# Kernel tuning notes

Hardware: AMD Instinct MI355X
Metric: run time of the kernel (lower is better)

The kernel has to match this reference:

```python
import jax, jax.numpy as jnp
import numpy as np

B, J, E, H = 32, 512, 512, 8
HD = E // H
EPS = 1e-7


def log_map0_spatial(x):
    # Lorentz log map at origin o=(1,0,...,0); return spatial (tangent) part.
    x0 = jnp.maximum(x[..., 0], 1.0 + 1e-7)      # [B,J]
    xs = x[..., 1:]                               # [B,J,E]
    nrm = jnp.linalg.norm(xs, axis=-1, keepdims=True)
    theta = jnp.arccosh(x0)[..., None]
    return theta * xs / jnp.maximum(nrm, EPS)


def exp_map0(v_s):
    # Lorentz exp map at origin of tangent vector (0, v_s) -> (cosh|v|, sinh|v| v/|v|).
    nrm = jnp.linalg.norm(v_s, axis=-1, keepdims=True)
    safe = jnp.maximum(nrm, EPS)
    return jnp.concatenate([jnp.cosh(nrm), jnp.sinh(nrm) * v_s / safe], axis=-1)


def setup_inputs() -> dict:
    key = jax.random.key(0)
    ks = jax.random.split(key, 8)
    xs = 0.5 * jax.random.normal(ks[0], (B, J, E), dtype=jnp.float32)
    x0 = jnp.sqrt(1.0 + jnp.sum(xs * xs, axis=-1, keepdims=True))  # valid hyperboloid
    x = jnp.concatenate([x0, xs], axis=-1)                          # [B,J,E+1]
    x_vel = jax.random.normal(ks[1], (B, J, E + 1), dtype=jnp.float32)
    topo_bias = 0.1 * jax.random.normal(ks[2], (J, J), dtype=jnp.float32)
    s = 1.0 / np.sqrt(E)
    W_qkv = jax.random.uniform(ks[3], (3 * E, E), jnp.float32, -s, s)
    W_vproj = jax.random.uniform(ks[4], (E, E), jnp.float32, -s, s)
    W_proj = jax.random.uniform(ks[5], (E, E), jnp.float32, -s, s)
    b_proj = jax.random.uniform(ks[6], (E,), jnp.float32, -s, s)
    return {"x": x, "x_vel": x_vel, "topo_bias": topo_bias,
            "W_qkv": W_qkv, "W_vproj": W_vproj, "W_proj": W_proj, "b_proj": b_proj}


def reference(x, x_vel, topo_bias, W_qkv, W_vproj, W_proj, b_proj):
    # Dropout is inference-mode (identity) for a deterministic reference.
    x_tan = log_map0_spatial(x)                                   # [B,J,E]
    v_tan = x_vel[..., 1:]                                        # [B,J,E]
    qkv = (x_tan @ W_qkv.T).reshape(B, J, 3, H, HD)
    qkv = jnp.transpose(qkv, (2, 0, 3, 1, 4))                     # [3,B,H,J,hd]
    q, k, v = qkv[0], qkv[1], qkv[2]
    k_vel = jnp.transpose((v_tan @ W_vproj.T).reshape(B, J, H, HD), (0, 2, 1, 3))
    k = k + k_vel
    scale = HD ** -0.5
    attn = jnp.einsum('bhqd,bhkd->bhqk', q, k) * scale + topo_bias[None, None]
    attn = jax.nn.softmax(attn, axis=-1)                          # [B,H,J,J]
    z_tan = jnp.einsum('bhqk,bhkd->bhqd', attn, v)
    z_tan = jnp.transpose(z_tan, (0, 2, 1, 3)).reshape(B, J, E)
    z_tan = z_tan @ W_proj.T + b_proj
    z_manifold = exp_map0(z_tan)                                  # [B,J,E+1]
    return (z_manifold, attn, x_tan)
```

## Files before the change

kernel.cpp:

```cpp
#include <hip/hip_runtime.h>
#include <hip/hip_bf16.h>
#include <math.h>

#define Jdim 512
#define Edim 512

typedef short short8 __attribute__((ext_vector_type(8)));
typedef float f32x4 __attribute__((ext_vector_type(4)));
typedef unsigned short u16;
typedef unsigned int u32;

__device__ __forceinline__ u16 f2b(float f) {
    union { float f; u32 u; } v; v.f = f;
    u32 r = (v.u + 0x7FFFu + ((v.u >> 16) & 1u)) >> 16;
    return (u16)r;
}
__device__ __forceinline__ float b2f(u16 u) {
    union { u32 u; float f; } v; v.u = ((u32)u) << 16;
    return v.f;
}

__device__ __forceinline__ void gl_lds16(const void* g, void* l) {
    __builtin_amdgcn_global_load_lds(
        (const __attribute__((address_space(1))) u32*)g,
        (__attribute__((address_space(3))) u32*)l, 16, 0, 0);
}

__global__ __launch_bounds__(256) void convw(
    const float* __restrict__ Wqkv, const float* __restrict__ Wvp,
    const float* __restrict__ Wproj,
    u16* __restrict__ Wq, u16* __restrict__ Wv, u16* __restrict__ Wp,
    u16* __restrict__ Wcat)
{
    int i = blockIdx.x * 256 + threadIdx.x;
    if (i < 262144) {
        Wq[i] = f2b(Wqkv[i]);
        Wv[i] = f2b(Wqkv[524288 + i]);
        Wp[i] = f2b(Wproj[i]);
    }
    int n = i >> 10, c = i & 1023;
    float v = (c < 512) ? Wqkv[(size_t)(512 + n) * 512 + c]
                        : Wvp[(size_t)n * 512 + (c - 512)];
    Wcat[i] = f2b(v);
}

__global__ __launch_bounds__(256) void xtan_kernel(
    const float* __restrict__ x, const float* __restrict__ xvel,
    float* __restrict__ xtan_out, u16* __restrict__ Acat)
{
    int row = blockIdx.x, tid = threadIdx.x;
    int lane = tid & 63, w = tid >> 6;
    const float* xr = x + (size_t)row * 513;
    float a0 = xr[1 + tid], a1 = xr[1 + tid + 256];
    float ss = a0 * a0 + a1 * a1;
    for (int o = 32; o >= 1; o >>= 1) ss += __shfl_down(ss, o);
    __shared__ float wsum[4];
    if (lane == 0) wsum[w] = ss;
    __syncthreads();
    float nrm = sqrtf(wsum[0] + wsum[1] + wsum[2] + wsum[3]);
    float x0 = fmaxf(xr[0], 1.0f + 1e-7f);
    float theta = acoshf(x0);
    float scl = theta / fmaxf(nrm, 1e-7f);
    float t0 = a0 * scl, t1 = a1 * scl;
    xtan_out[(size_t)row * 512 + tid] = t0;
    xtan_out[(size_t)row * 512 + tid + 256] = t1;
    u16* ac = Acat + (size_t)row * 1024;
    ac[tid] = f2b(t0);
    ac[tid + 256] = f2b(t1);
    const float* vr = xvel + (size_t)row * 513;
    ac[512 + tid] = f2b(vr[1 + tid]);
    ac[768 + tid] = f2b(vr[1 + tid + 256]);
}

__global__ __launch_bounds__(256) void gemm_qkv(
    const u16* __restrict__ A,
    const u16* __restrict__ Wq, const u16* __restrict__ Wcat,
    const u16* __restrict__ Wv,
    u16* __restrict__ qbuf, u16* __restrict__ kbuf, u16* __restrict__ vbuf)
{
    __shared__ u16 As[128 * 64];
    __shared__ u16 Bs[128 * 64];
    const int tid = threadIdx.x;
    const int w = tid >> 6, lane = tid & 63, l15 = lane & 15, quad = lane >> 4;
    const int m0 = blockIdx.y * 128;
    const int n0g = blockIdx.x * 128;
    const int seg = n0g >> 9;
    const int n0 = n0g & 511;
    const u16* Bm; int ldb, K; u16* outb;
    if (seg == 0)      { Bm = Wq;   ldb = 512;  K = 512;  outb = qbuf; }
    else if (seg == 1) { Bm = Wcat; ldb = 1024; K = 1024; outb = kbuf; }
    else               { Bm = Wv;   ldb = 512;  K = 512;  outb = vbuf; }
    const int wm = (w & 1) * 64, wn = (w >> 1) * 64;

    f32x4 acc[4][4];
#pragma unroll
    for (int i = 0; i < 4; i++)
#pragma unroll
        for (int j = 0; j < 4; j++) acc[i][j] = (f32x4)0.0f;

    for (int kt = 0; kt < K; kt += 64) {
#pragma unroll
        for (int i = 0; i < 4; i++) {
            int c = i * 256 + tid;
            int row = c >> 3, s = c & 7, gc = s ^ (row & 7);
            gl_lds16(&A[(size_t)(m0 + row) * 1024 + kt + gc * 8],
                     &As[(size_t)(i * 256 + (tid & ~63)) * 8]);
        }
#pragma unroll
        for (int i = 0; i < 4; i++) {
            int c = i * 256 + tid;
            int row = c >> 3, s = c & 7, gc = s ^ (row & 7);
            gl_lds16(&Bm[(size_t)(n0 + row) * ldb + kt + gc * 8],
                     &Bs[(size_t)(i * 256 + (tid & ~63)) * 8]);
        }
        __syncthreads();
#pragma unroll
        for (int kc = 0; kc < 2; kc++) {
            short8 af[4], bf[4];
#pragma unroll
            for (int t = 0; t < 4; t++) {
                int row = wm + t * 16 + l15;
                int slot = (kc * 4 + quad) ^ (row & 7);
                af[t] = *(const short8*)&As[row * 64 + slot * 8];
            }
#pragma unroll
            for (int t = 0; t < 4; t++) {
                int row = wn + t * 16 + l15;
                int slot = (kc * 4 + quad) ^ (row & 7);
                bf[t] = *(const short8*)&Bs[row * 64 + slot * 8];
            }
#pragma unroll
            for (int ti = 0; ti < 4; ti++)
#pragma unroll
                for (int tj = 0; tj < 4; tj++)
                    acc[ti][tj] = __builtin_amdgcn_mfma_f32_16x16x32_bf16(
                        af[ti], bf[tj], acc[ti][tj], 0, 0, 0);
        }
        __syncthreads();
    }

#pragma unroll
    for (int ti = 0; ti < 4; ti++)
#pragma unroll
        for (int tj = 0; tj < 4; tj++)
#pragma unroll
            for (int r = 0; r < 4; r++) {
                int gm = m0 + wm + ti * 16 + quad * 4 + r;
                int gn = n0 + wn + tj * 16 + l15;
                int b = gm >> 9, j = gm & 511, h = gn >> 6, d = gn & 63;
                outb[(((size_t)(b * 8 + h) * 512 + j) << 6) + d] = f2b(acc[ti][tj][r]);
            }
}

__global__ __launch_bounds__(256) void gemm_proj(
    const u16* __restrict__ A, int lda,
    const u16* __restrict__ Bm, int ldb, int K,
    float* __restrict__ out_f, const float* __restrict__ bias)
{
    __shared__ u16 As[128 * 64];
    __shared__ u16 Bs[128 * 64];
    const int tid = threadIdx.x;
    const int w = tid >> 6, lane = tid & 63, l15 = lane & 15, quad = lane >> 4;
    const int m0 = blockIdx.y * 128, n0 = blockIdx.x * 128;
    const int wm = (w & 1) * 64, wn = (w >> 1) * 64;

    f32x4 acc[4][4];
#pragma unroll
    for (int i = 0; i < 4; i++)
#pragma unroll
        for (int j = 0; j < 4; j++) acc[i][j] = (f32x4)0.0f;

    for (int kt = 0; kt < K; kt += 64) {
#pragma unroll
        for (int i = 0; i < 4; i++) {
            int c = i * 256 + tid;
            int row = c >> 3, s = c & 7, gc = s ^ (row & 7);
            gl_lds16(&A[(size_t)(m0 + row) * lda + kt + gc * 8],
                     &As[(size_t)(i * 256 + (tid & ~63)) * 8]);
        }
#pragma unroll
        for (int i = 0; i < 4; i++) {
            int c = i * 256 + tid;
            int row = c >> 3, s = c & 7, gc = s ^ (row & 7);
            gl_lds16(&Bm[(size_t)(n0 + row) * ldb + kt + gc * 8],
                     &Bs[(size_t)(i * 256 + (tid & ~63)) * 8]);
        }
        __syncthreads();
#pragma unroll
        for (int kc = 0; kc < 2; kc++) {
            short8 af[4], bf[4];
#pragma unroll
            for (int t = 0; t < 4; t++) {
                int row = wm + t * 16 + l15;
                int slot = (kc * 4 + quad) ^ (row & 7);
                af[t] = *(const short8*)&As[row * 64 + slot * 8];
            }
#pragma unroll
            for (int t = 0; t < 4; t++) {
                int row = wn + t * 16 + l15;
                int slot = (kc * 4 + quad) ^ (row & 7);
                bf[t] = *(const short8*)&Bs[row * 64 + slot * 8];
            }
#pragma unroll
            for (int ti = 0; ti < 4; ti++)
#pragma unroll
                for (int tj = 0; tj < 4; tj++)
                    acc[ti][tj] = __builtin_amdgcn_mfma_f32_16x16x32_bf16(
                        af[ti], bf[tj], acc[ti][tj], 0, 0, 0);
        }
        __syncthreads();
    }

#pragma unroll
    for (int ti = 0; ti < 4; ti++)
#pragma unroll
        for (int tj = 0; tj < 4; tj++)
#pragma unroll
            for (int r = 0; r < 4; r++) {
                int gm = m0 + wm + ti * 16 + quad * 4 + r;
                int gn = n0 + wn + tj * 16 + l15;
                out_f[(size_t)gm * 512 + gn] = acc[ti][tj][r] + bias[gn];
            }
}

__global__ __launch_bounds__(256) void vtrans(
    const u16* __restrict__ vb, u16* __restrict__ vT)
{
    __shared__ u16 tile[64][65];
    int bh = blockIdx.x >> 3, jt = blockIdx.x & 7;
    const u16* src = vb + (size_t)bh * 512 * 64 + (size_t)jt * 64 * 64;
#pragma unroll
    for (int i = 0; i < 16; i++) {
        int e = i * 256 + threadIdx.x;
        tile[e >> 6][e & 63] = src[e];
    }
    __syncthreads();
    u16* dst = vT + (size_t)bh * 64 * 512 + jt * 64;
#pragma unroll
    for (int i = 0; i < 16; i++) {
        int e = i * 256 + threadIdx.x;
        int d = e >> 6, jj = e & 63;
        dst[(size_t)d * 512 + jj] = tile[jj][d];
    }
}

__global__ __launch_bounds__(256) void attn_kernel(
    const u16* __restrict__ qb, const u16* __restrict__ kb,
    const u16* __restrict__ vT, const float* __restrict__ bias,
    float* __restrict__ attn_out, u16* __restrict__ z_bf)
{
    __shared__ u16 Sb[32 * 520];
    __shared__ float row_m[32], row_is[32];
    const int tid = threadIdx.x, w = tid >> 6, lane = tid & 63;
    const int l15 = lane & 15, quad = lane >> 4;
    const int bh = blockIdx.x >> 4, qt = blockIdx.x & 15;
    const int q0 = qt * 32;
    const u16* qp = qb + (size_t)bh * 512 * 64;
    const u16* kp = kb + (size_t)bh * 512 * 64;

    short8 qf[2][2];
#pragma unroll
    for (int ti = 0; ti < 2; ti++)
#pragma unroll
        for (int kc = 0; kc < 2; kc++)
            qf[ti][kc] = *(const short8*)&qp[(q0 + ti * 16 + l15) * 64 + kc * 32 + quad * 8];

    f32x4 sacc[2][8];
#pragma unroll
    for (int ti = 0; ti < 2; ti++)
#pragma unroll
        for (int kt = 0; kt < 8; kt++) sacc[ti][kt] = (f32x4)0.0f;

    const int kbase = w * 128;
#pragma unroll
    for (int kt = 0; kt < 8; kt++) {
        short8 kf[2];
        int n = kbase + kt * 16 + l15;
#pragma unroll
        for (int kc = 0; kc < 2; kc++)
            kf[kc] = *(const short8*)&kp[n * 64 + kc * 32 + quad * 8];
#pragma unroll
        for (int ti = 0; ti < 2; ti++)
#pragma unroll
            for (int kc = 0; kc < 2; kc++)
                sacc[ti][kt] = __builtin_amdgcn_mfma_f32_16x16x32_bf16(
                    qf[ti][kc], kf[kc], sacc[ti][kt], 0, 0, 0);
    }
#pragma unroll
    for (int ti = 0; ti < 2; ti++)
#pragma unroll
        for (int kt = 0; kt < 8; kt++) {
            int col = kbase + kt * 16 + l15;
#pragma unroll
            for (int r = 0; r < 4; r++) {
                int row = ti * 16 + quad * 4 + r;
                float s = sacc[ti][kt][r] * 0.125f +
                          bias[(size_t)(q0 + row) * 512 + col];
                Sb[row * 520 + col] = f2b(s);
            }
        }
    __syncthreads();

    {
        int srow = tid >> 3, li = tid & 7;
        const u16* srp = &Sb[srow * 520];
        float m = -1e30f;
#pragma unroll
        for (int t = 0; t < 16; t++) {
            uint2 sv = *(const uint2*)&srp[(li + 8 * t) * 4];
            float m01 = fmaxf(b2f((u16)(sv.x & 0xffff)), b2f((u16)(sv.x >> 16)));
            float m23 = fmaxf(b2f((u16)(sv.y & 0xffff)), b2f((u16)(sv.y >> 16)));
            m = fmaxf(m, fmaxf(m01, m23));
        }
        m = fmaxf(m, __shfl_xor(m, 1));
        m = fmaxf(m, __shfl_xor(m, 2));
        m = fmaxf(m, __shfl_xor(m, 4));
        if (li == 0) row_m[srow] = m;
        float sum = 0.0f;
#pragma unroll
        for (int t = 0; t < 16; t++) {
            uint2 sv = *(const uint2*)&srp[(li + 8 * t) * 4];
            sum += __expf(b2f((u16)(sv.x & 0xffff)) - m)
                 + __expf(b2f((u16)(sv.x >> 16)) - m)
                 + __expf(b2f((u16)(sv.y & 0xffff)) - m)
                 + __expf(b2f((u16)(sv.y >> 16)) - m);
        }
        sum += __shfl_xor(sum, 1);
        sum += __shfl_xor(sum, 2);
        sum += __shfl_xor(sum, 4);
        if (li == 0) row_is[srow] = 1.0f / sum;
        __syncthreads();
    }

    float* attn_p = attn_out + (size_t)bh * 512 * 512 + (size_t)q0 * 512;
#pragma unroll
    for (int i = 0; i < 16; i++) {
        int e = i * 256 + tid;
        int row = e >> 7, cq = (e & 127) * 4;
        uint2 sv = *(const uint2*)&Sb[row * 520 + cq];
        float m = row_m[row], is = row_is[row];
        float p0 = __expf(b2f((u16)(sv.x & 0xffff)) - m) * is;
        float p1 = __expf(b2f((u16)(sv.x >> 16)) - m) * is;
        float p2 = __expf(b2f((u16)(sv.y & 0xffff)) - m) * is;
        float p3 = __expf(b2f((u16)(sv.y >> 16)) - m) * is;
        f32x4 pv; pv[0] = p0; pv[1] = p1; pv[2] = p2; pv[3] = p3;
        *(f32x4*)&attn_p[(size_t)row * 512 + cq] = pv;
        uint2 pk;
        pk.x = (u32)f2b(p0) | ((u32)f2b(p1) << 16);
        pk.y = (u32)f2b(p2) | ((u32)f2b(p3) << 16);
        *(uint2*)&Sb[row * 520 + cq] = pk;
    }
    __syncthreads();

    const u16* vp = vT + (size_t)bh * 64 * 512;
    f32x4 zacc[2];
    zacc[0] = (f32x4)0.0f; zacc[1] = (f32x4)0.0f;
    int n0 = w * 16;
#pragma unroll
    for (int kc = 0; kc < 16; kc++) {
        short8 bfv = *(const short8*)&vp[(size_t)(n0 + l15) * 512 + kc * 32 + quad * 8];
#pragma unroll
        for (int ti = 0; ti < 2; ti++) {
            short8 afp = *(const short8*)&Sb[(ti * 16 + l15) * 520 + kc * 32 + quad * 8];
            zacc[ti] = __builtin_amdgcn_mfma_f32_16x16x32_bf16(afp, bfv, zacc[ti], 0, 0, 0);
        }
    }
    int b = bh >> 3, h = bh & 7;
#pragma unroll
    for (int ti = 0; ti < 2; ti++)
#pragma unroll
        for (int r = 0; r < 4; r++) {
            int row = q0 + ti * 16 + quad * 4 + r;
            int d = n0 + l15;
            z_bf[((size_t)b * 512 + row) * 512 + h * 64 + d] = f2b(zacc[ti][r]);
        }
}

__global__ __launch_bounds__(256) void expmap_kernel(
    const float* __restrict__ zp, float* __restrict__ out0)
{
    int row = blockIdx.x, tid = threadIdx.x;
    int lane = tid & 63, w = tid >> 6;
    const float* zr = zp + (size_t)row * 512;
    float a0 = zr[tid], a1 = zr[tid + 256];
    float ss = a0 * a0 + a1 * a1;
    for (int o = 32; o >= 1; o >>= 1) ss += __shfl_down(ss, o);
    __shared__ float wsum[4];
    if (lane == 0) wsum[w] = ss;
    __syncthreads();
    float nrm = sqrtf(wsum[0] + wsum[1] + wsum[2] + wsum[3]);
    float scl = sinhf(nrm) / fmaxf(nrm, 1e-7f);
    float* orow = out0 + (size_t)row * 513;
    if (tid == 0) orow[0] = coshf(nrm);
    orow[1 + tid] = a0 * scl;
    orow[1 + tid + 256] = a1 * scl;
}

extern "C" void kernel_launch(void* const* d_in, const int* in_sizes, int n_in,
                              void* d_out, int out_size, void* d_ws, size_t ws_size,
                              hipStream_t stream) {
    const float* x     = (const float*)d_in[0];
    const float* xvel  = (const float*)d_in[1];
    const float* topo  = (const float*)d_in[2];
    const float* Wqkv  = (const float*)d_in[3];
    const float* Wvp   = (const float*)d_in[4];
    const float* Wproj = (const float*)d_in[5];
    const float* bproj = (const float*)d_in[6];

    float* out      = (float*)d_out;
    float* out_zman = out;
    float* out_attn = out + 8404992;
    float* out_xtan = out + 75513856;

    char* ws = (char*)d_ws;
    u16*   Acat  = (u16*)ws;
    u16*   Wq    = (u16*)(ws + 33554432);
    u16*   Wv    = (u16*)(ws + 34078720);
    u16*   Wp    = (u16*)(ws + 34603008);
    u16*   Wcat  = (u16*)(ws + 35127296);
    u16*   qbuf  = (u16*)(ws + 36175872);
    u16*   kbuf  = (u16*)(ws + 52953088);
    u16*   vbuf  = (u16*)(ws + 69730304);
    u16*   vT    = (u16*)(ws + 86507520);
    u16*   zbf   = (u16*)(ws + 103284736);
    float* zproj = (float*)(ws + 120061952);

    convw<<<2048, 256, 0, stream>>>(Wqkv, Wvp, Wproj, Wq, Wv, Wp, Wcat);
    xtan_kernel<<<16384, 256, 0, stream>>>(x, xvel, out_xtan, Acat);

    dim3 gq(12, 128);
    gemm_qkv<<<gq, 256, 0, stream>>>(Acat, Wq, Wcat, Wv, qbuf, kbuf, vbuf);

    vtrans<<<2048, 256, 0, stream>>>(vbuf, vT);

    attn_kernel<<<4096, 256, 0, stream>>>(qbuf, kbuf, vT, topo, out_attn, zbf);

    dim3 g(4, 128);
    gemm_proj<<<g, 256, 0, stream>>>(zbf, 512, Wp, 512, 512, zproj, bproj);
    expmap_kernel<<<16384, 256, 0, stream>>>(zproj, out_zman);
}
```

Measured before the change: 560.3 us.

## Fuse V transpose into QKV GEMM epilogue and simplify softmax normalization

The QKV GEMM epilogue now stages its output tile in LDS and writes coalesced 16-byte vectors. The V segment is written already transposed, so the separate vtrans kernel and its extra pass over V are gone. In attention, the exponentials are computed once and stored unnormalized in LDS, and the 1/sum scale is applied both to the fp32 attn output and after the PV MMA. This removes the second exp pass and one barrier, and the z output is staged through LDS for vectorized stores. Numerics change slightly because the unnormalized exponentials are rounded to bf16 before the PV product.

```diff
diff --git a/kernel.cpp b/kernel.cpp
--- a/kernel.cpp
+++ b/kernel.cpp
@@ -76,10 +76,11 @@
     const u16* __restrict__ A,
     const u16* __restrict__ Wq, const u16* __restrict__ Wcat,
     const u16* __restrict__ Wv,
-    u16* __restrict__ qbuf, u16* __restrict__ kbuf, u16* __restrict__ vbuf)
-{
-    __shared__ u16 As[128 * 64];
-    __shared__ u16 Bs[128 * 64];
+    u16* __restrict__ qbuf, u16* __restrict__ kbuf, u16* __restrict__ vT)
+{
+    __shared__ u16 smem[16384];
+    u16* As = smem;
+    u16* Bs = smem + 8192;
     const int tid = threadIdx.x;
     const int w = tid >> 6, lane = tid & 63, l15 = lane & 15, quad = lane >> 4;
     const int m0 = blockIdx.y * 128;
@@ -89,7 +90,7 @@
     const u16* Bm; int ldb, K; u16* outb;
     if (seg == 0)      { Bm = Wq;   ldb = 512;  K = 512;  outb = qbuf; }
     else if (seg == 1) { Bm = Wcat; ldb = 1024; K = 1024; outb = kbuf; }
-    else               { Bm = Wv;   ldb = 512;  K = 512;  outb = vbuf; }
+    else               { Bm = Wv;   ldb = 512;  K = 512;  outb = vT;   }
     const int wm = (w & 1) * 64, wn = (w >> 1) * 64;
 
     f32x4 acc[4][4];
@@ -139,17 +140,54 @@
         __syncthreads();
     }
 
-#pragma unroll
-    for (int ti = 0; ti < 4; ti++)
-#pragma unroll
-        for (int tj = 0; tj < 4; tj++)
-#pragma unroll
-            for (int r = 0; r < 4; r++) {
-                int gm = m0 + wm + ti * 16 + quad * 4 + r;
-                int gn = n0 + wn + tj * 16 + l15;
-                int b = gm >> 9, j = gm & 511, h = gn >> 6, d = gn & 63;
-                outb[(((size_t)(b * 8 + h) * 512 + j) << 6) + d] = f2b(acc[ti][tj][r]);
-            }
+    const int b = m0 >> 9, jb = m0 & 511, h0 = n0 >> 6;
+    if (seg < 2) {
+#pragma unroll
+        for (int ti = 0; ti < 4; ti++)
+#pragma unroll
+            for (int tj = 0; tj < 4; tj++)
+#pragma unroll
+                for (int r = 0; r < 4; r++) {
+                    int row = wm + ti * 16 + quad * 4 + r;
+                    int col = wn + tj * 16 + l15;
+                    int g = (col >> 3) ^ (row & 7);
+                    smem[row * 128 + g * 8 + (col & 7)] = f2b(acc[ti][tj][r]);
+                }
+        __syncthreads();
+#pragma unroll
+        for (int hh = 0; hh < 2; hh++) {
+            u16* obase = outb + (((size_t)(b * 8 + h0 + hh) * 512 + jb) << 6);
+#pragma unroll
+            for (int p = 0; p < 4; p++) {
+                int jrow = p * 32 + (tid >> 3);
+                int grp = (hh * 8 + (tid & 7)) ^ (jrow & 7);
+                short8 vv = *(const short8*)&smem[jrow * 128 + grp * 8];
+                *(short8*)&obase[jrow * 64 + (tid & 7) * 8] = vv;
+            }
+        }
+    } else {
+#pragma unroll
+        for (int ti = 0; ti < 4; ti++)
+#pragma unroll
+            for (int tj = 0; tj < 4; tj++)
+#pragma unroll
+                for (int r = 0; r < 4; r++) {
+                    int row = wm + ti * 16 + quad * 4 + r;
+                    int col = wn + tj * 16 + l15;
+                    int g = (row >> 3) ^ (col & 15);
+                    smem[col * 128 + g * 8 + (row & 7)] = f2b(acc[ti][tj][r]);
+                }
+        __syncthreads();
+#pragma unroll
+        for (int p = 0; p < 8; p++) {
+            int d = p * 16 + (tid >> 4);
+            int j0 = (tid & 15) * 8;
+            int g = (j0 >> 3) ^ (d & 15);
+            short8 vv = *(const short8*)&smem[d * 128 + g * 8];
+            int h = h0 + (d >> 6), dg = d & 63;
+            *(short8*)&outb[(((size_t)(b * 8 + h) << 6) + dg) * 512 + jb + j0] = vv;
+        }
+    }
 }
 
 __global__ __launch_bounds__(256) void gemm_proj(
@@ -223,34 +261,13 @@
             }
 }
 
-__global__ __launch_bounds__(256) void vtrans(
-    const u16* __restrict__ vb, u16* __restrict__ vT)
-{
-    __shared__ u16 tile[64][65];
-    int bh = blockIdx.x >> 3, jt = blockIdx.x & 7;
-    const u16* src = vb + (size_t)bh * 512 * 64 + (size_t)jt * 64 * 64;
-#pragma unroll
-    for (int i = 0; i < 16; i++) {
-        int e = i * 256 + threadIdx.x;
-        tile[e >> 6][e & 63] = src[e];
-    }
-    __syncthreads();
-    u16* dst = vT + (size_t)bh * 64 * 512 + jt * 64;
-#pragma unroll
-    for (int i = 0; i < 16; i++) {
-        int e = i * 256 + threadIdx.x;
-        int d = e >> 6, jj = e & 63;
-        dst[(size_t)d * 512 + jj] = tile[jj][d];
-    }
-}
-
 __global__ __launch_bounds__(256) void attn_kernel(
     const u16* __restrict__ qb, const u16* __restrict__ kb,
     const u16* __restrict__ vT, const float* __restrict__ bias,
     float* __restrict__ attn_out, u16* __restrict__ z_bf)
 {
     __shared__ u16 Sb[32 * 520];
-    __shared__ float row_m[32], row_is[32];
+    __shared__ float row_is[32];
     const int tid = threadIdx.x, w = tid >> 6, lane = tid & 63;
     const int l15 = lane & 15, quad = lane >> 4;
     const int bh = blockIdx.x >> 4, qt = blockIdx.x & 15;
@@ -303,7 +320,7 @@
 
     {
         int srow = tid >> 3, li = tid & 7;
-        const u16* srp = &Sb[srow * 520];
+        u16* srp = &Sb[srow * 520];
         float m = -1e30f;
 #pragma unroll
         for (int t = 0; t < 16; t++) {
@@ -315,22 +332,26 @@
         m = fmaxf(m, __shfl_xor(m, 1));
         m = fmaxf(m, __shfl_xor(m, 2));
         m = fmaxf(m, __shfl_xor(m, 4));
-        if (li == 0) row_m[srow] = m;
         float sum = 0.0f;
 #pragma unroll
         for (int t = 0; t < 16; t++) {
             uint2 sv = *(const uint2*)&srp[(li + 8 * t) * 4];
-            sum += __expf(b2f((u16)(sv.x & 0xffff)) - m)
-                 + __expf(b2f((u16)(sv.x >> 16)) - m)
-                 + __expf(b2f((u16)(sv.y & 0xffff)) - m)
-                 + __expf(b2f((u16)(sv.y >> 16)) - m);
+            float e0 = __expf(b2f((u16)(sv.x & 0xffff)) - m);
+            float e1 = __expf(b2f((u16)(sv.x >> 16)) - m);
+            float e2 = __expf(b2f((u16)(sv.y & 0xffff)) - m);
+            float e3 = __expf(b2f((u16)(sv.y >> 16)) - m);
+            sum += (e0 + e1) + (e2 + e3);
+            uint2 pk;
+            pk.x = (u32)f2b(e0) | ((u32)f2b(e1) << 16);
+            pk.y = (u32)f2b(e2) | ((u32)f2b(e3) << 16);
+            *(uint2*)&srp[(li + 8 * t) * 4] = pk;
         }
         sum += __shfl_xor(sum, 1);
         sum += __shfl_xor(sum, 2);
         sum += __shfl_xor(sum, 4);
         if (li == 0) row_is[srow] = 1.0f / sum;
-        __syncthreads();
-    }
+    }
+    __syncthreads();
 
     float* attn_p = attn_out + (size_t)bh * 512 * 512 + (size_t)q0 * 512;
 #pragma unroll
@@ -338,19 +359,14 @@
         int e = i * 256 + tid;
         int row = e >> 7, cq = (e & 127) * 4;
         uint2 sv = *(const uint2*)&Sb[row * 520 + cq];
-        float m = row_m[row], is = row_is[row];
-        float p0 = __expf(b2f((u16)(sv.x & 0xffff)) - m) * is;
-        float p1 = __expf(b2f((u16)(sv.x >> 16)) - m) * is;
-        float p2 = __expf(b2f((u16)(sv.y & 0xffff)) - m) * is;
-        float p3 = __expf(b2f((u16)(sv.y >> 16)) - m) * is;
-        f32x4 pv; pv[0] = p0; pv[1] = p1; pv[2] = p2; pv[3] = p3;
+        float is = row_is[row];
+        f32x4 pv;
+        pv[0] = b2f((u16)(sv.x & 0xffff)) * is;
+        pv[1] = b2f((u16)(sv.x >> 16)) * is;
+        pv[2] = b2f((u16)(sv.y & 0xffff)) * is;
+        pv[3] = b2f((u16)(sv.y >> 16)) * is;
         *(f32x4*)&attn_p[(size_t)row * 512 + cq] = pv;
-        uint2 pk;
-        pk.x = (u32)f2b(p0) | ((u32)f2b(p1) << 16);
-        pk.y = (u32)f2b(p2) | ((u32)f2b(p3) << 16);
-        *(uint2*)&Sb[row * 520 + cq] = pk;
-    }
-    __syncthreads();
+    }
 
     const u16* vp = vT + (size_t)bh * 64 * 512;
     f32x4 zacc[2];
@@ -365,15 +381,24 @@
             zacc[ti] = __builtin_amdgcn_mfma_f32_16x16x32_bf16(afp, bfv, zacc[ti], 0, 0, 0);
         }
     }
-    int b = bh >> 3, h = bh & 7;
+    __syncthreads();
+
+    u16* Zs = Sb;
 #pragma unroll
     for (int ti = 0; ti < 2; ti++)
 #pragma unroll
         for (int r = 0; r < 4; r++) {
-            int row = q0 + ti * 16 + quad * 4 + r;
-            int d = n0 + l15;
-            z_bf[((size_t)b * 512 + row) * 512 + h * 64 + d] = f2b(zacc[ti][r]);
-        }
+            int rl = ti * 16 + quad * 4 + r;
+            Zs[rl * 64 + n0 + l15] = f2b(zacc[ti][r] * row_is[rl]);
+        }
+    __syncthreads();
+
+    {
+        int rl = tid >> 3, dblk = (tid & 7) * 8;
+        short8 zv = *(const short8*)&Zs[rl * 64 + dblk];
+        int b = bh >> 3, h = bh & 7;
+        *(short8*)&z_bf[((size_t)(b * 512 + q0 + rl) * 512) + h * 64 + dblk] = zv;
+    }
 }
 
 __global__ __launch_bounds__(256) void expmap_kernel(
@@ -420,7 +445,6 @@
     u16*   Wcat  = (u16*)(ws + 35127296);
     u16*   qbuf  = (u16*)(ws + 36175872);
     u16*   kbuf  = (u16*)(ws + 52953088);
-    u16*   vbuf  = (u16*)(ws + 69730304);
     u16*   vT    = (u16*)(ws + 86507520);
     u16*   zbf   = (u16*)(ws + 103284736);
     float* zproj = (float*)(ws + 120061952);
@@ -429,9 +453,7 @@
     xtan_kernel<<<16384, 256, 0, stream>>>(x, xvel, out_xtan, Acat);
 
     dim3 gq(12, 128);
-    gemm_qkv<<<gq, 256, 0, stream>>>(Acat, Wq, Wcat, Wv, qbuf, kbuf, vbuf);
-
-    vtrans<<<2048, 256, 0, stream>>>(vbuf, vT);
+    gemm_qkv<<<gq, 256, 0, stream>>>(Acat, Wq, Wcat, Wv, qbuf, kbuf, vT);
 
     attn_kernel<<<4096, 256, 0, stream>>>(qbuf, kbuf, vT, topo, out_attn, zbf);
 
```

Result: slower. 619.8 us (+10.6%).
